# Optimization experiments

Hardware: AMD Instinct MI355X
Metric: run time of the kernel (lower is better)

## Reference

```python
import jax, jax.numpy as jnp
import numpy as np

S, B, I, H = 512, 64, 1024, 1024


def setup_inputs() -> dict:
    key = jax.random.key(0)
    ks = jax.random.split(key, 6)
    std = 1.0 / np.sqrt(H)
    inp = {
        "input_": jax.random.normal(ks[0], (S, B, I), dtype=jnp.float32),
        "h0": jnp.zeros((B, H), dtype=jnp.float32),
        "c0": jnp.zeros((B, H), dtype=jnp.float32),
        "weight_ih": jax.random.uniform(ks[1], (4 * H, I), jnp.float32, -std, std),
        "weight_hh": jax.random.uniform(ks[2], (4 * H, H), jnp.float32, -std, std),
        "bias_ih": jax.random.uniform(ks[3], (4 * H,), jnp.float32, -std, std),
        "bias_hh": jax.random.uniform(ks[4], (4 * H,), jnp.float32, -std, std),
        # reset_parameters() re-initializes ALL params uniform(-std, std), incl. retention_ratio
        "retention_ratio": jax.random.uniform(ks[5], (H,), jnp.float32, -std, std),
    }
    return inp


def _lstm_scan(input_, h0, c0, weight_ih, weight_hh, bias_ih, bias_hh, retention_ratio):
    # Precompute input projections for all timesteps: [S, B, 4H]
    x_gates = jnp.einsum("sbi,gi->sbg", input_, weight_ih) + bias_ih + bias_hh
    r = retention_ratio

    def step(carry, xg):
        hx, cx = carry
        gates = xg + hx @ weight_hh.T  # [B, 4H]
        i, f, g, o = jnp.split(gates, 4, axis=1)
        i = jax.nn.sigmoid(i)
        f = jax.nn.sigmoid(f)
        g = jnp.tanh(g)
        o = jax.nn.sigmoid(o)
        cy = f * cx + i * g
        hy = o * jnp.tanh(cy)
        hy = r * hx + (1.0 - r) * hy  # low-pass retention filter
        return (hy, cy), hy

    (h, c), outputs = jax.lax.scan(step, (h0, c0), x_gates)
    return outputs, (h, c)


def reference(input_, h0, c0, weight_ih, weight_hh, bias_ih, bias_hh, retention_ratio):
    outputs, (h, c) = _lstm_scan(input_, h0, c0, weight_ih, weight_hh,
                                 bias_ih, bias_hh, retention_ratio)
    # th.squeeze(th.stack(outputs)) is a no-op for S,B,H > 1
    return outputs, (h, c)
```

## Files before the change

kernel.cpp:

```cpp
#include <hip/hip_runtime.h>
#include <hip/hip_bf16.h>
#include <cstdint>

#define S_LEN 512
#define BATCH 64
#define IDIM  1024
#define HDIM  1024
#define G4    4096
#define NBLK  256

typedef __attribute__((ext_vector_type(8))) short short8;
typedef __attribute__((ext_vector_type(8))) unsigned short ushort8;
typedef __attribute__((ext_vector_type(4))) float f32x4;
typedef __attribute__((ext_vector_type(4))) unsigned short ushort4v;
typedef __attribute__((ext_vector_type(4))) unsigned int uint4v;

__device__ __forceinline__ unsigned short f2bf(float f){
  union { float f; unsigned u; } v; v.f = f;
  unsigned r = (v.u + 0x7fffu + ((v.u >> 16) & 1u)) >> 16;
  return (unsigned short)r;
}
__device__ __forceinline__ float bf2f(unsigned short s){
  union { unsigned u; float f; } v; v.u = ((unsigned)s) << 16;
  return v.f;
}
__device__ __forceinline__ float sigf(float x){ return 1.0f / (1.0f + __expf(-x)); }
__device__ __forceinline__ float tanhf_fast(float x){
  float e = __expf(2.0f * x);
  return 1.0f - 2.0f / (e + 1.0f);
}
__device__ __forceinline__ f32x4 mfma_bf16(short8 a, short8 b, f32x4 c){
  return __builtin_amdgcn_mfma_f32_16x16x32_bf16(a, b, c, 0, 0, 0);
}

__device__ __forceinline__ void load8_bypass(const unsigned short* p, short8* d){
  asm volatile(
    "global_load_dwordx4 %0, %8, off sc0 sc1\n\t"
    "global_load_dwordx4 %1, %8, off offset:64 sc0 sc1\n\t"
    "global_load_dwordx4 %2, %8, off offset:128 sc0 sc1\n\t"
    "global_load_dwordx4 %3, %8, off offset:192 sc0 sc1\n\t"
    "global_load_dwordx4 %4, %8, off offset:256 sc0 sc1\n\t"
    "global_load_dwordx4 %5, %8, off offset:320 sc0 sc1\n\t"
    "global_load_dwordx4 %6, %8, off offset:384 sc0 sc1\n\t"
    "global_load_dwordx4 %7, %8, off offset:448 sc0 sc1\n\t"
    "s_waitcnt vmcnt(0)"
    : "=&v"(d[0]), "=&v"(d[1]), "=&v"(d[2]), "=&v"(d[3]),
      "=&v"(d[4]), "=&v"(d[5]), "=&v"(d[6]), "=&v"(d[7])
    : "v"(p)
    : "memory");
}
__device__ __forceinline__ void store_short_bypass(unsigned short* p, unsigned v){
  asm volatile("global_store_short %0, %1, off sc0 sc1" :: "v"(p), "v"(v) : "memory");
}
__device__ __forceinline__ void store_dword_bypass(unsigned* p, unsigned v){
  asm volatile("global_store_dword %0, %1, off sc0 sc1" :: "v"(p), "v"(v) : "memory");
}
__device__ __forceinline__ uint4v load4_flags_bypass(const unsigned* p){
  uint4v f;
  asm volatile("global_load_dwordx4 %0, %1, off sc0 sc1\n\ts_waitcnt vmcnt(0)"
               : "=&v"(f) : "v"(p) : "memory");
  return f;
}

__global__ __launch_bounds__(256) void convert_kernel(
    const float* __restrict__ In, unsigned short* __restrict__ InB){
  size_t i = ((size_t)blockIdx.x * 256 + threadIdx.x) * 4;
  f32x4 v = *reinterpret_cast<const f32x4*>(&In[i]);
  ushort4v u; u[0]=f2bf(v[0]); u[1]=f2bf(v[1]); u[2]=f2bf(v[2]); u[3]=f2bf(v[3]);
  *reinterpret_cast<ushort4v*>(&InB[i]) = u;
}

__global__ __launch_bounds__(256) void prep_kernel(
    const float* __restrict__ Whh, const float* __restrict__ Wih,
    const float* __restrict__ bih, const float* __restrict__ bhh,
    const float* __restrict__ h0, unsigned short* __restrict__ WpackHH,
    unsigned short* __restrict__ WpackIH, float* __restrict__ biasSum,
    unsigned short* __restrict__ hA){
  int i = blockIdx.x * 256 + threadIdx.x;
  if (i < G4) biasSum[i] = bih[i] + bhh[i];
  if (i < BATCH*HDIM) hA[i] = f2bf(h0[i]);
  int p = (i < G4*HDIM) ? i : i - G4*HDIM;
  int e = p & 7, l = (p >> 3) & 63, ks = (p >> 9) & 7;
  int gate = (p >> 12) & 3, w = (p >> 14) & 3, cb = p >> 16;
  int row = gate * HDIM + cb * 16 + (l & 15);
  int k = w * 256 + ks * 32 + (l >> 4) * 8 + e;
  if (i < G4*HDIM) WpackHH[p] = f2bf(Whh[row * HDIM + k]);
  else             WpackIH[p] = f2bf(Wih[row * IDIM + k]);
}

__global__ __launch_bounds__(256, 1) void recur_kernel(
    const float* __restrict__ h0, const float* __restrict__ c0,
    const float* __restrict__ ret, const unsigned short* __restrict__ WpackHH,
    const unsigned short* __restrict__ WpackIH, const unsigned short* __restrict__ InB,
    const float* __restrict__ biasSum, unsigned short* __restrict__ hA,
    unsigned short* __restrict__ hB, float* __restrict__ out,
    float* __restrict__ hc_out, unsigned* __restrict__ flags){
  __shared__ __align__(16) float partA[5120];
  __shared__ __align__(16) float partB[5120];

  const int bid = blockIdx.x;
  const int cb = bid & 63, g = bid >> 6;
  const int tid = threadIdx.x;
  const int w = tid >> 6, l = tid & 63;
  const int lm = l & 15, lq = l >> 4;

  short8 WfH[4][8], WfI[4][8];
  {
    const short8* wph = reinterpret_cast<const short8*>(WpackHH)
                      + (size_t)(cb * 4 + w) * 2048 + l;
    const short8* wpi = reinterpret_cast<const short8*>(WpackIH)
                      + (size_t)(cb * 4 + w) * 2048 + l;
    #pragma unroll
    for (int gate = 0; gate < 4; ++gate)
      #pragma unroll
      for (int ks = 0; ks < 8; ++ks){
        WfH[gate][ks] = wph[(gate * 8 + ks) * 64];
        WfI[gate][ks] = wpi[(gate * 8 + ks) * 64];
      }
  }

  const int bl = tid >> 4, j = tid & 15;
  const int bglob = g * 16 + bl, jglob = cb * 16 + j;
  float c_reg = c0[bglob * HDIM + jglob];
  float h_reg = h0[bglob * HDIM + jglob];
  float r_reg = ret[jglob];
  float bias_reg[4];
  #pragma unroll
  for (int gate = 0; gate < 4; ++gate)
    bias_reg[gate] = biasSum[gate * 1024 + jglob];

  const size_t in_off = (size_t)(g * 16 + lm) * 1024 + w * 256 + lq * 8;

  unsigned* gflags = flags + g * 1024;

  float xv[4];
  {
    short8 inr0[8];
    const short8* ip = reinterpret_cast<const short8*>(InB + in_off);
    #pragma unroll
    for (int ks = 0; ks < 8; ++ks) inr0[ks] = ip[ks * 4];
    f32x4 accI[4];
    #pragma unroll
    for (int gate = 0; gate < 4; ++gate) accI[gate] = (f32x4){0.f,0.f,0.f,0.f};
    #pragma unroll
    for (int ks = 0; ks < 8; ++ks)
      #pragma unroll
      for (int gate = 0; gate < 4; ++gate)
        accI[gate] = mfma_bf16(inr0[ks], WfI[gate][ks], accI[gate]);
    #pragma unroll
    for (int r = 0; r < 4; ++r){
      f32x4 vB = (f32x4){accI[0][r], accI[1][r], accI[2][r], accI[3][r]};
      *reinterpret_cast<f32x4*>(&partB[((lq * 4 + r) * 16 + lm) * 20 + w * 4]) = vB;
    }
    __syncthreads();
    f32x4 s0 = (f32x4){bias_reg[0], bias_reg[1], bias_reg[2], bias_reg[3]};
    #pragma unroll
    for (int ww = 0; ww < 4; ++ww)
      s0 += *reinterpret_cast<const f32x4*>(&partB[tid * 20 + ww * 4]);
    xv[0] = s0[0]; xv[1] = s0[1]; xv[2] = s0[2]; xv[3] = s0[3];
    __syncthreads();
  }

  short8 inr[8];
  {
    const short8* ip = reinterpret_cast<const short8*>(InB + 65536 + in_off);
    #pragma unroll
    for (int ks = 0; ks < 8; ++ks) inr[ks] = ip[ks * 4];
  }

  for (int s = 0; s < S_LEN; ++s){
    const unsigned short* cur = (s & 1) ? hB : hA;
    unsigned short* nxt = (s & 1) ? hA : hB;

    const unsigned short* hp = cur + (size_t)(g * 16 + lm) * HDIM + w * 256 + lq * 8;
    short8 hr[8];
    load8_bypass(hp, hr);

    f32x4 accH[4], accI[4];
    #pragma unroll
    for (int gate = 0; gate < 4; ++gate){
      accH[gate] = (f32x4){0.f,0.f,0.f,0.f};
      accI[gate] = (f32x4){0.f,0.f,0.f,0.f};
    }
    #pragma unroll
    for (int ks = 0; ks < 8; ++ks){
      accH[0] = mfma_bf16(hr[ks], WfH[0][ks], accH[0]);
      accH[1] = mfma_bf16(hr[ks], WfH[1][ks], accH[1]);
      accH[2] = mfma_bf16(hr[ks], WfH[2][ks], accH[2]);
      accH[3] = mfma_bf16(hr[ks], WfH[3][ks], accH[3]);
      accI[0] = mfma_bf16(inr[ks], WfI[0][ks], accI[0]);
      accI[1] = mfma_bf16(inr[ks], WfI[1][ks], accI[1]);
      accI[2] = mfma_bf16(inr[ks], WfI[2][ks], accI[2]);
      accI[3] = mfma_bf16(inr[ks], WfI[3][ks], accI[3]);
    }

    #pragma unroll
    for (int r = 0; r < 4; ++r){
      int a = ((lq * 4 + r) * 16 + lm) * 20 + w * 4;
      f32x4 vA = (f32x4){accH[0][r], accH[1][r], accH[2][r], accH[3][r]};
      f32x4 vB = (f32x4){accI[0][r], accI[1][r], accI[2][r], accI[3][r]};
      *reinterpret_cast<f32x4*>(&partA[a]) = vA;
      *reinterpret_cast<f32x4*>(&partB[a]) = vB;
    }
    __syncthreads();

    f32x4 gs = (f32x4){xv[0], xv[1], xv[2], xv[3]};
    #pragma unroll
    for (int ww = 0; ww < 4; ++ww)
      gs += *reinterpret_cast<const f32x4*>(&partA[tid * 20 + ww * 4]);
    float ig = sigf(gs[0]), fg = sigf(gs[1]);
    float gt = tanhf_fast(gs[2]), og = sigf(gs[3]);
    float cy = fg * c_reg + ig * gt;
    float hy = og * tanhf_fast(cy);
    hy = r_reg * h_reg + (1.0f - r_reg) * hy;
    c_reg = cy; h_reg = hy;
    store_short_bypass(&nxt[bglob * HDIM + jglob], (unsigned)f2bf(hy));

    asm volatile("s_waitcnt vmcnt(0)" ::: "memory");
    const unsigned tgt = (unsigned)(s + 1);
    if (l == 0)
      store_dword_bypass(&gflags[cb * 16 + w], tgt);

    {
      f32x4 sB = (f32x4){bias_reg[0], bias_reg[1], bias_reg[2], bias_reg[3]};
      #pragma unroll
      for (int ww = 0; ww < 4; ++ww)
        sB += *reinterpret_cast<const f32x4*>(&partB[tid * 20 + ww * 4]);
      xv[0] = sB[0]; xv[1] = sB[1]; xv[2] = sB[2]; xv[3] = sB[3];
    }

    const int sn = (s + 2 < S_LEN) ? s + 2 : S_LEN - 1;
    const short8* ipn = reinterpret_cast<const short8*>(InB + (size_t)sn * 65536 + in_off);
    if (w == 0){
      const unsigned* fp = gflags + (l << 4);
      unsigned spins = 0;
      for (;;){
        uint4v f = load4_flags_bypass(fp);
        if (f[0] >= tgt && f[1] >= tgt && f[2] >= tgt && f[3] >= tgt) break;
        __builtin_amdgcn_s_sleep(1);
        if (++spins > 50000000u) break;
      }
      #pragma unroll
      for (int ks = 0; ks < 8; ++ks) inr[ks] = ipn[ks * 4];
    } else {
      #pragma unroll
      for (int ks = 0; ks < 8; ++ks) inr[ks] = ipn[ks * 4];
    }
    __syncthreads();

    out[((size_t)s * BATCH + bglob) * HDIM + jglob] = h_reg;
  }

  hc_out[bglob * HDIM + jglob] = h_reg;
  hc_out[BATCH * HDIM + bglob * HDIM + jglob] = c_reg;
}

extern "C" void kernel_launch(void* const* d_in, const int* in_sizes, int n_in,
                              void* d_out, int out_size, void* d_ws, size_t ws_size,
                              hipStream_t stream){
  const float* In  = (const float*)d_in[0];
  const float* h0  = (const float*)d_in[1];
  const float* c0  = (const float*)d_in[2];
  const float* Wih = (const float*)d_in[3];
  const float* Whh = (const float*)d_in[4];
  const float* bih = (const float*)d_in[5];
  const float* bhh = (const float*)d_in[6];
  const float* ret = (const float*)d_in[7];
  float* out = (float*)d_out;

  char* ws = (char*)d_ws;
  const size_t off_flags = 0;
  const size_t off_bias  = 16384;
  const size_t off_hA    = 32768;
  const size_t off_hB    = off_hA + 131072;
  const size_t off_wph   = off_hB + 131072;
  const size_t off_wpi   = off_wph + 8388608;
  const size_t off_inb   = off_wpi + 8388608;
  const size_t need      = off_inb + 67108864;

  unsigned*       flags   = (unsigned*)(ws + off_flags);
  float*          biasSum = (float*)(ws + off_bias);
  unsigned short* hA      = (unsigned short*)(ws + off_hA);
  unsigned short* hB      = (unsigned short*)(ws + off_hB);
  unsigned short* WpackHH = (unsigned short*)(ws + off_wph);
  unsigned short* WpackIH = (unsigned short*)(ws + off_wpi);
  unsigned short* InB     = (unsigned short*)(ws + off_inb);

  if (ws_size < need) return;

  (void)hipMemsetAsync(ws + off_flags, 0, 16384, stream);
  convert_kernel<<<32768, 256, 0, stream>>>(In, InB);
  prep_kernel<<<32768, 256, 0, stream>>>(Whh, Wih, bih, bhh, h0,
                                         WpackHH, WpackIH, biasSum, hA);

  float* hc_out = out + (size_t)S_LEN * BATCH * HDIM;
  recur_kernel<<<NBLK, 256, 0, stream>>>(h0, c0, ret, WpackHH, WpackIH, InB,
                                         biasSum, hA, hB, out, hc_out, flags);
}
```

Before: 2.529 ms.

## Fuse fp32-to-bf16 input conversion into recurrent kernel with async prefetch

```diff
diff --git a/kernel.cpp b/kernel.cpp
--- a/kernel.cpp
+++ b/kernel.cpp
@@ -31,6 +31,15 @@
 }
 __device__ __forceinline__ f32x4 mfma_bf16(short8 a, short8 b, f32x4 c){
   return __builtin_amdgcn_mfma_f32_16x16x32_bf16(a, b, c, 0, 0, 0);
+}
+
+__device__ __forceinline__ short8 cvt8(f32x4 a, f32x4 b){
+  union { unsigned u[4]; short8 s; } r;
+  asm("v_cvt_pk_bf16_f32 %0, %1, %2" : "=v"(r.u[0]) : "v"(a[0]), "v"(a[1]));
+  asm("v_cvt_pk_bf16_f32 %0, %1, %2" : "=v"(r.u[1]) : "v"(a[2]), "v"(a[3]));
+  asm("v_cvt_pk_bf16_f32 %0, %1, %2" : "=v"(r.u[2]) : "v"(b[0]), "v"(b[1]));
+  asm("v_cvt_pk_bf16_f32 %0, %1, %2" : "=v"(r.u[3]) : "v"(b[2]), "v"(b[3]));
+  return r.s;
 }
 
 __device__ __forceinline__ void load8_bypass(const unsigned short* p, short8* d){
@@ -49,6 +58,31 @@
     : "v"(p)
     : "memory");
 }
+__device__ __forceinline__ void load16f_nowait(const float* p, f32x4* d){
+  asm volatile(
+    "global_load_dwordx4 %0, %16, off\n\t"
+    "global_load_dwordx4 %1, %16, off offset:16\n\t"
+    "global_load_dwordx4 %2, %16, off offset:128\n\t"
+    "global_load_dwordx4 %3, %16, off offset:144\n\t"
+    "global_load_dwordx4 %4, %16, off offset:256\n\t"
+    "global_load_dwordx4 %5, %16, off offset:272\n\t"
+    "global_load_dwordx4 %6, %16, off offset:384\n\t"
+    "global_load_dwordx4 %7, %16, off offset:400\n\t"
+    "global_load_dwordx4 %8, %16, off offset:512\n\t"
+    "global_load_dwordx4 %9, %16, off offset:528\n\t"
+    "global_load_dwordx4 %10, %16, off offset:640\n\t"
+    "global_load_dwordx4 %11, %16, off offset:656\n\t"
+    "global_load_dwordx4 %12, %16, off offset:768\n\t"
+    "global_load_dwordx4 %13, %16, off offset:784\n\t"
+    "global_load_dwordx4 %14, %16, off offset:896\n\t"
+    "global_load_dwordx4 %15, %16, off offset:912"
+    : "=&v"(d[0]), "=&v"(d[1]), "=&v"(d[2]), "=&v"(d[3]),
+      "=&v"(d[4]), "=&v"(d[5]), "=&v"(d[6]), "=&v"(d[7]),
+      "=&v"(d[8]), "=&v"(d[9]), "=&v"(d[10]), "=&v"(d[11]),
+      "=&v"(d[12]), "=&v"(d[13]), "=&v"(d[14]), "=&v"(d[15])
+    : "v"(p)
+    : "memory");
+}
 __device__ __forceinline__ void store_short_bypass(unsigned short* p, unsigned v){
   asm volatile("global_store_short %0, %1, off sc0 sc1" :: "v"(p), "v"(v) : "memory");
 }
@@ -60,14 +94,6 @@
   asm volatile("global_load_dwordx4 %0, %1, off sc0 sc1\n\ts_waitcnt vmcnt(0)"
                : "=&v"(f) : "v"(p) : "memory");
   return f;
-}
-
-__global__ __launch_bounds__(256) void convert_kernel(
-    const float* __restrict__ In, unsigned short* __restrict__ InB){
-  size_t i = ((size_t)blockIdx.x * 256 + threadIdx.x) * 4;
-  f32x4 v = *reinterpret_cast<const f32x4*>(&In[i]);
-  ushort4v u; u[0]=f2bf(v[0]); u[1]=f2bf(v[1]); u[2]=f2bf(v[2]); u[3]=f2bf(v[3]);
-  *reinterpret_cast<ushort4v*>(&InB[i]) = u;
 }
 
 __global__ __launch_bounds__(256) void prep_kernel(
@@ -91,7 +117,7 @@
 __global__ __launch_bounds__(256, 1) void recur_kernel(
     const float* __restrict__ h0, const float* __restrict__ c0,
     const float* __restrict__ ret, const unsigned short* __restrict__ WpackHH,
-    const unsigned short* __restrict__ WpackIH, const unsigned short* __restrict__ InB,
+    const unsigned short* __restrict__ WpackIH, const float* __restrict__ In,
     const float* __restrict__ biasSum, unsigned short* __restrict__ hA,
     unsigned short* __restrict__ hB, float* __restrict__ out,
     float* __restrict__ hc_out, unsigned* __restrict__ flags){
@@ -135,18 +161,17 @@
 
   float xv[4];
   {
-    short8 inr0[8];
-    const short8* ip = reinterpret_cast<const short8*>(InB + in_off);
-    #pragma unroll
-    for (int ks = 0; ks < 8; ++ks) inr0[ks] = ip[ks * 4];
+    const f32x4* fp0 = reinterpret_cast<const f32x4*>(In + in_off);
     f32x4 accI[4];
     #pragma unroll
     for (int gate = 0; gate < 4; ++gate) accI[gate] = (f32x4){0.f,0.f,0.f,0.f};
     #pragma unroll
-    for (int ks = 0; ks < 8; ++ks)
+    for (int ks = 0; ks < 8; ++ks){
+      short8 in8 = cvt8(fp0[ks * 8], fp0[ks * 8 + 1]);
       #pragma unroll
       for (int gate = 0; gate < 4; ++gate)
-        accI[gate] = mfma_bf16(inr0[ks], WfI[gate][ks], accI[gate]);
+        accI[gate] = mfma_bf16(in8, WfI[gate][ks], accI[gate]);
+    }
     #pragma unroll
     for (int r = 0; r < 4; ++r){
       f32x4 vB = (f32x4){accI[0][r], accI[1][r], accI[2][r], accI[3][r]};
@@ -161,20 +186,33 @@
     __syncthreads();
   }
 
-  short8 inr[8];
+  f32x4 fpre[16];
   {
-    const short8* ip = reinterpret_cast<const short8*>(InB + 65536 + in_off);
-    #pragma unroll
-    for (int ks = 0; ks < 8; ++ks) inr[ks] = ip[ks * 4];
+    const f32x4* fp1 = reinterpret_cast<const f32x4*>(In + 65536 + in_off);
+    #pragma unroll
+    for (int ks = 0; ks < 8; ++ks){
+      fpre[2 * ks]     = fp1[ks * 8];
+      fpre[2 * ks + 1] = fp1[ks * 8 + 1];
+    }
   }
 
   for (int s = 0; s < S_LEN; ++s){
     const unsigned short* cur = (s & 1) ? hB : hA;
     unsigned short* nxt = (s & 1) ? hA : hB;
 
+    short8 inr[8];
+    #pragma unroll
+    for (int ks = 0; ks < 8; ++ks)
+      inr[ks] = cvt8(fpre[2 * ks], fpre[2 * ks + 1]);
+
     const unsigned short* hp = cur + (size_t)(g * 16 + lm) * HDIM + w * 256 + lq * 8;
     short8 hr[8];
     load8_bypass(hp, hr);
+
+    {
+      const int sn = (s + 2 < S_LEN) ? s + 2 : S_LEN - 1;
+      load16f_nowait(In + (size_t)sn * 65536 + in_off, fpre);
+    }
 
     f32x4 accH[4], accI[4];
     #pragma unroll
@@ -229,8 +267,6 @@
       xv[0] = sB[0]; xv[1] = sB[1]; xv[2] = sB[2]; xv[3] = sB[3];
     }
 
-    const int sn = (s + 2 < S_LEN) ? s + 2 : S_LEN - 1;
-    const short8* ipn = reinterpret_cast<const short8*>(InB + (size_t)sn * 65536 + in_off);
     if (w == 0){
       const unsigned* fp = gflags + (l << 4);
       unsigned spins = 0;
@@ -240,11 +276,6 @@
         __builtin_amdgcn_s_sleep(1);
         if (++spins > 50000000u) break;
       }
-      #pragma unroll
-      for (int ks = 0; ks < 8; ++ks) inr[ks] = ipn[ks * 4];
-    } else {
-      #pragma unroll
-      for (int ks = 0; ks < 8; ++ks) inr[ks] = ipn[ks * 4];
     }
     __syncthreads();
 
@@ -275,8 +306,7 @@
   const size_t off_hB    = off_hA + 131072;
   const size_t off_wph   = off_hB + 131072;
   const size_t off_wpi   = off_wph + 8388608;
-  const size_t off_inb   = off_wpi + 8388608;
-  const size_t need      = off_inb + 67108864;
+  const size_t need      = off_wpi + 8388608;
 
   unsigned*       flags   = (unsigned*)(ws + off_flags);
   float*          biasSum = (float*)(ws + off_bias);
@@ -284,16 +314,14 @@
   unsigned short* hB      = (unsigned short*)(ws + off_hB);
   unsigned short* WpackHH = (unsigned short*)(ws + off_wph);
   unsigned short* WpackIH = (unsigned short*)(ws + off_wpi);
-  unsigned short* InB     = (unsigned short*)(ws + off_inb);
 
   if (ws_size < need) return;
 
   (void)hipMemsetAsync(ws + off_flags, 0, 16384, stream);
-  convert_kernel<<<32768, 256, 0, stream>>>(In, InB);
   prep_kernel<<<32768, 256, 0, stream>>>(Whh, Wih, bih, bhh, h0,
                                          WpackHH, WpackIH, biasSum, hA);
 
   float* hc_out = out + (size_t)S_LEN * BATCH * HDIM;
-  recur_kernel<<<NBLK, 256, 0, stream>>>(h0, c0, ret, WpackHH, WpackIH, InB,
+  recur_kernel<<<NBLK, 256, 0, stream>>>(h0, c0, ret, WpackHH, WpackIH, In,
                                          biasSum, hA, hB, out, hc_out, flags);
 }
```

Result: slower. 2.642 ms (+4.5%).
